# Kernel optimization log

Hardware: AMD Instinct MI355X
Metric: run time of the kernel (lower is better)

## Reference

```python
import jax, jax.numpy as jnp
import numpy as np
from jax import lax

EPS = 1e-5  # BatchNorm eps (torch default)

def _up2_bilinear_ac(x):
    # bilinear upsample x2, align_corners=True; x: [B,C,H,W]
    B, C, H, W = x.shape
    def axis_interp(n_in, n_out):
        pos = jnp.arange(n_out, dtype=jnp.float32) * ((n_in - 1) / (n_out - 1))
        i0 = jnp.floor(pos).astype(jnp.int32)
        i1 = jnp.minimum(i0 + 1, n_in - 1)
        w = (pos - i0.astype(jnp.float32)).astype(x.dtype)
        return i0, i1, w
    i0, i1, wh = axis_interp(H, 2 * H)
    x = x[:, :, i0, :] * (1.0 - wh)[None, None, :, None] + x[:, :, i1, :] * wh[None, None, :, None]
    j0, j1, ww = axis_interp(W, 2 * W)
    x = x[:, :, :, j0] * (1.0 - ww) + x[:, :, :, j1] * ww
    return x

def setup_inputs() -> dict:
    key = jax.random.key(0)
    ks = jax.random.split(key, 8)
    B, Cin, Cout, H, W = 8, 64, 32, 128, 128
    att, K = 16, 2  # attention_channel = max(int(64*0.0625),16)=16; kernel_num=2
    n = lambda k, s, sc: jax.random.normal(k, s, jnp.float32) * sc
    return {
        'x': n(ks[0], (B, Cin, H, W), 1.0),
        'fc_w': n(ks[1], (att, Cin), 0.1),
        'bn_a_gamma': jnp.ones((att,), jnp.float32), 'bn_a_beta': jnp.zeros((att,), jnp.float32),
        'bn_a_mean': jnp.zeros((att,), jnp.float32), 'bn_a_var': jnp.ones((att,), jnp.float32),
        'ch_w': n(ks[2], (Cin, att), 0.1), 'ch_b': jnp.zeros((Cin,), jnp.float32),
        'fil_w': n(ks[3], (Cout, att), 0.1), 'fil_b': jnp.zeros((Cout,), jnp.float32),
        'sp_w': n(ks[4], (9, att), 0.1), 'sp_b': jnp.zeros((9,), jnp.float32),
        'k_w': n(ks[5], (K, att), 0.1), 'k_b': jnp.zeros((K,), jnp.float32),
        'weight': n(ks[6], (K, Cout, Cin, 3, 3), 0.05),
        'bn_gamma': jnp.ones((Cout,), jnp.float32), 'bn_beta': jnp.zeros((Cout,), jnp.float32),
        'bn_mean': jnp.zeros((Cout,), jnp.float32), 'bn_var': jnp.ones((Cout,), jnp.float32),
    }

def reference(x, fc_w, bn_a_gamma, bn_a_beta, bn_a_mean, bn_a_var,
              ch_w, ch_b, fil_w, fil_b, sp_w, sp_b, k_w, k_b,
              weight, bn_gamma, bn_beta, bn_mean, bn_var):
    x = _up2_bilinear_ac(x)
    B, Cin, H, W = x.shape
    K, Cout = weight.shape[0], weight.shape[1]
    # --- ODConv attention branch (on GAP features) ---
    g = x.mean(axis=(2, 3))                                    # [B,Cin]
    h = g @ fc_w.T                                             # [B,att]
    h = (h - bn_a_mean) / jnp.sqrt(bn_a_var + EPS) * bn_a_gamma + bn_a_beta
    h = jax.nn.relu(h)
    ch_att = jax.nn.sigmoid(h @ ch_w.T + ch_b)                 # [B,Cin]
    fil_att = jax.nn.sigmoid(h @ fil_w.T + fil_b)              # [B,Cout]
    sp_att = jax.nn.sigmoid(h @ sp_w.T + sp_b).reshape(B, 1, 1, 1, 3, 3)
    k_att = jax.nn.softmax(h @ k_w.T + k_b, axis=1).reshape(B, K, 1, 1, 1, 1)
    # per-sample aggregated filters: [B,Cout,Cin,3,3]
    agg_w = jnp.sum(k_att * sp_att * weight[None], axis=1)
    # --- dynamic conv (per-sample filter), channel-attended input ---
    x = x * ch_att[:, :, None, None]
    def conv1(xi, wi):
        return lax.conv_general_dilated(xi[None], wi, (1, 1), [(1, 1), (1, 1)],
                                        dimension_numbers=('NCHW', 'OIHW', 'NCHW'))[0]
    y = jax.vmap(conv1)(x, agg_w)                              # [B,Cout,H,W]
    y = y * fil_att[:, :, None, None]
    # --- BatchNorm2d (inference) + GELU (exact erf) ---
    y = (y - bn_mean[:, None, None]) / jnp.sqrt(bn_var[:, None, None] + EPS)
    y = y * bn_gamma[:, None, None] + bn_beta[:, None, None]
    return jax.nn.gelu(y, approximate=False)
```

## Files before the change

kernel.cpp:

```cpp
#include <hip/hip_runtime.h>
#include <hip/hip_bf16.h>

#define EPSBN 1e-5f

typedef short short8 __attribute__((ext_vector_type(8)));
typedef float f32x16 __attribute__((ext_vector_type(16)));

static __device__ __forceinline__ unsigned short f2u(float f){
  __hip_bfloat16 h = __float2bfloat16(f);
  union { __hip_bfloat16 h; unsigned short u; } c; c.h = h; return c.u;
}

#define WS_WR    0
#define WS_G     2048
#define WS_CH    4096
#define WS_SP    6144
#define WS_KA    6656
#define WS_S     7168
#define WS_T     8192
#define WS_AGGB  16384
#define WS_XUP   327680

__global__ void k_wr(float* __restrict__ wr){
  int i = threadIdx.x;
  float s = 0.f;
  for (int r = 0; r < 256; ++r){
    float pos = (float)r * (127.0f/255.0f);
    int i0 = (int)pos; float w = pos - (float)i0; int i1 = min(i0+1,127);
    if (i0 == i) s += 1.0f - w;
    if (i1 == i) s += w;
  }
  wr[i] = s;
}

__global__ void k_gap(const float* __restrict__ x, const float* __restrict__ wr,
                      float* __restrict__ g){
  __shared__ float w[128];
  __shared__ float partial[4];
  int tid = threadIdx.x;
  if (tid < 128) w[tid] = wr[tid];
  __syncthreads();
  const float* xp = x + ((size_t)blockIdx.x << 14);
  float s = 0.f;
  for (int idx = tid; idx < 16384; idx += 256){
    int i = idx >> 7, j = idx & 127;
    s += xp[idx] * w[i] * w[j];
  }
  for (int off = 32; off > 0; off >>= 1) s += __shfl_down(s, off, 64);
  if ((tid & 63) == 0) partial[tid >> 6] = s;
  __syncthreads();
  if (tid == 0) g[blockIdx.x] = (partial[0]+partial[1]+partial[2]+partial[3]) * (1.0f/65536.0f);
}

__global__ void k_att(const float* __restrict__ g,
                      const float* __restrict__ fc_w,
                      const float* __restrict__ bga, const float* __restrict__ bba,
                      const float* __restrict__ bma, const float* __restrict__ bva,
                      const float* __restrict__ ch_w, const float* __restrict__ ch_b,
                      const float* __restrict__ fil_w, const float* __restrict__ fil_b,
                      const float* __restrict__ sp_w, const float* __restrict__ sp_b,
                      const float* __restrict__ k_w, const float* __restrict__ k_b,
                      const float* __restrict__ bn_g, const float* __restrict__ bn_b,
                      const float* __restrict__ bn_m, const float* __restrict__ bn_v,
                      float* __restrict__ ch_att, float* __restrict__ sp_att,
                      float* __restrict__ k_att_o, float* __restrict__ sS, float* __restrict__ tT)
{
  __shared__ float h[8][16];
  int tid = threadIdx.x;
  if (tid < 128){
    int b = tid >> 4, a = tid & 15;
    float acc = 0.f;
    for (int c = 0; c < 64; ++c) acc += g[b*64+c] * fc_w[a*64+c];
    float v = (acc - bma[a]) * rsqrtf(bva[a] + EPSBN) * bga[a] + bba[a];
    h[b][a] = fmaxf(v, 0.f);
  }
  __syncthreads();
  for (int i = tid; i < 512; i += 256){
    int b = i >> 6, c = i & 63;
    float z = ch_b[c];
    for (int a = 0; a < 16; ++a) z += h[b][a]*ch_w[c*16+a];
    ch_att[i] = 1.f/(1.f+expf(-z));
  }
  {
    int b = tid >> 5, o = tid & 31;
    float z = fil_b[o];
    for (int a = 0; a < 16; ++a) z += h[b][a]*fil_w[o*16+a];
    float f = 1.f/(1.f+expf(-z));
    float inv = rsqrtf(bn_v[o] + EPSBN);
    sS[tid] = f * bn_g[o] * inv;
    if (b == 0) tT[o] = bn_b[o] - bn_m[o] * bn_g[o] * inv;
  }
  if (tid < 72){
    int b = tid / 9, s = tid % 9;
    float z = sp_b[s];
    for (int a = 0; a < 16; ++a) z += h[b][a]*sp_w[s*16+a];
    sp_att[tid] = 1.f/(1.f+expf(-z));
  }
  if (tid < 8){
    int b = tid;
    float z0 = k_b[0], z1 = k_b[1];
    for (int a = 0; a < 16; ++a){ z0 += h[b][a]*k_w[a]; z1 += h[b][a]*k_w[16+a]; }
    float m = fmaxf(z0, z1);
    float e0 = expf(z0-m), e1 = expf(z1-m), inv = 1.f/(e0+e1);
    k_att_o[b*2]   = e0*inv;
    k_att_o[b*2+1] = e1*inv;
  }
}

__global__ void k_aggw(const float* __restrict__ weight, const float* __restrict__ ch_att,
                       const float* __restrict__ sp_att, const float* __restrict__ ka,
                       unsigned short* __restrict__ aggb)
{
  int idx = blockIdx.x*256 + threadIdx.x;
  int ci_l = idx & 15;
  int o    = (idx >> 4) & 31;
  int s    = (idx >> 9) % 9;
  int t2   = idx / 4608;
  int cc   = t2 & 3, b = t2 >> 2;
  int ci   = cc*16 + ci_l;
  float w0 = weight[(o*64+ci)*9+s];
  float w1 = weight[((32+o)*64+ci)*9+s];
  float v  = ch_att[b*64+ci] * sp_att[b*9+s] * (ka[b*2]*w0 + ka[b*2+1]*w1);
  aggb[idx] = f2u(v);
}

__global__ __launch_bounds__(256) void k_up(const float* __restrict__ x,
                                            unsigned int* __restrict__ xup32)
{
  __shared__ float xin[16*6*133];
  int tid = threadIdx.x;
  int bi  = blockIdx.x;
  int strip = bi & 31, cc = (bi >> 5) & 3, b = bi >> 7;
  int r0 = strip * 8;
  int i0b = (int)((float)r0 * (127.0f/255.0f));

  for (int e = tid; e < 12288; e += 256){
    int ir = e >> 11;
    int rem = e & 2047;
    int ci = rem >> 7;
    int j  = rem & 127;
    int row = min(i0b + ir, 127);
    xin[ci*798 + ir*133 + j] = x[(((size_t)(b*64 + cc*16 + ci)) << 14) + (row << 7) + j];
  }
  __syncthreads();

  for (int e2 = tid; e2 < 16384; e2 += 256){
    int ci2 = e2 & 7;
    int c   = (e2 >> 3) & 255;
    int rr  = e2 >> 11;
    int r   = r0 + rr;
    float posr = (float)r * (127.0f/255.0f);
    int i0g = (int)posr; float wh = posr - (float)i0g;
    int i1g = min(i0g+1, 127);
    int ir0 = i0g - i0b, ir1 = i1g - i0b;
    float posc = (float)c * (127.0f/255.0f);
    int j0 = (int)posc; float ww = posc - (float)j0;
    int j1 = min(j0+1, 127);
    unsigned int pack = 0;
    #pragma unroll
    for (int u = 0; u < 2; ++u){
      int ci = ci2*2 + u;
      const float* base = &xin[ci*798];
      float v00 = base[ir0*133 + j0], v01 = base[ir0*133 + j1];
      float v10 = base[ir1*133 + j0], v11 = base[ir1*133 + j1];
      float a0 = v00 + (v01 - v00)*ww;
      float a1 = v10 + (v11 - v10)*ww;
      float v  = a0 + (a1 - a0)*wh;
      pack |= ((unsigned int)f2u(v)) << (16*u);
    }
    size_t idx = ((((size_t)(b*4+cc)*256 + r)*256 + c) << 4) + ci2*2;
    xup32[idx >> 1] = pack;
  }
}

__global__ __launch_bounds__(256) void k_conv(const unsigned short* __restrict__ xup,
                                              const unsigned short* __restrict__ aggb,
                                              const float* __restrict__ sS,
                                              const float* __restrict__ tT,
                                              float* __restrict__ out)
{
  __shared__ unsigned short xt[18*18*24];
  __shared__ unsigned short wt[288*24];
  __shared__ float sSs[32], tTs[32];

  int tid = threadIdx.x;
  int bi  = blockIdx.x;
  int b   = bi >> 8, t = bi & 255;
  int p0  = (t >> 4) * 16, q0 = (t & 15) * 16;
  int lane = tid & 63, wv = tid >> 6;
  if (tid < 32){ sSs[tid] = sS[b*32+tid]; tTs[tid] = tT[tid]; }

  f32x16 acc[2];
  #pragma unroll
  for (int i = 0; i < 16; ++i){ acc[0][i] = 0.f; acc[1][i] = 0.f; }

  int n  = lane & 31;
  int kq = lane >> 5;

  for (int cc = 0; cc < 4; ++cc){
    if (cc) __syncthreads();
    for (int e = tid; e < 648; e += 256){
      int rr  = e / 36;
      int rem = e - rr*36;
      int qq  = rem >> 1;
      int half= rem & 1;
      int gr = p0 - 1 + rr, gq = q0 - 1 + qq;
      short8 v = {0,0,0,0,0,0,0,0};
      if ((unsigned)gr < 256u && (unsigned)gq < 256u){
        size_t gidx = ((((size_t)(b*4+cc)*256 + gr)*256 + gq) << 4) + half*8;
        v = *(const short8*)&xup[gidx];
      }
      *(short8*)&xt[(rr*18+qq)*24 + half*8] = v;
    }
    for (int e = tid; e < 576; e += 256){
      int so = e >> 1, half = e & 1;
      size_t gidx = (((size_t)(b*4+cc)*288 + so) << 4) + half*8;
      *(short8*)&wt[so*24 + half*8] = *(const short8*)&aggb[gidx];
    }
    __syncthreads();

    #pragma unroll
    for (int s = 0; s < 9; ++s){
      const int ky = s / 3, kx = s % 3;
      short8 av = *(const short8*)&wt[(s*32 + n)*24 + kq*8];
      #pragma unroll
      for (int tt = 0; tt < 2; ++tt){
        int lr = 2*(2*wv + tt) + (n >> 4);
        int rr = lr + ky;
        int qq = (n & 15) + kx;
        short8 bv = *(const short8*)&xt[(rr*18+qq)*24 + kq*8];
        acc[tt] = __builtin_amdgcn_mfma_f32_32x32x16_bf16(av, bv, acc[tt], 0, 0, 0);
      }
    }
  }

  #pragma unroll
  for (int tt = 0; tt < 2; ++tt){
    int lr = 2*(2*wv + tt) + (n >> 4);
    int p = p0 + lr, q = q0 + (n & 15);
    #pragma unroll
    for (int r = 0; r < 16; ++r){
      int o = (r & 3) + 8*(r >> 2) + 4*kq;
      float val = acc[tt][r]*sSs[o] + tTs[o];
      float gl  = 0.5f*val*(1.f + erff(val*0.70710678118f));
      out[(((size_t)(b*32+o)) << 16) + (p << 8) + q] = gl;
    }
  }
}

extern "C" void kernel_launch(void* const* d_in, const int* in_sizes, int n_in,
                              void* d_out, int out_size, void* d_ws, size_t ws_size,
                              hipStream_t stream)
{
  const float* x     = (const float*)d_in[0];
  const float* fc_w  = (const float*)d_in[1];
  const float* bga   = (const float*)d_in[2];
  const float* bba   = (const float*)d_in[3];
  const float* bma   = (const float*)d_in[4];
  const float* bva   = (const float*)d_in[5];
  const float* ch_w  = (const float*)d_in[6];
  const float* ch_b  = (const float*)d_in[7];
  const float* fil_w = (const float*)d_in[8];
  const float* fil_b = (const float*)d_in[9];
  const float* sp_w  = (const float*)d_in[10];
  const float* sp_b  = (const float*)d_in[11];
  const float* k_w   = (const float*)d_in[12];
  const float* k_b   = (const float*)d_in[13];
  const float* weight= (const float*)d_in[14];
  const float* bn_g  = (const float*)d_in[15];
  const float* bn_b  = (const float*)d_in[16];
  const float* bn_m  = (const float*)d_in[17];
  const float* bn_v  = (const float*)d_in[18];

  char* ws = (char*)d_ws;
  float* wr  = (float*)(ws + WS_WR);
  float* g   = (float*)(ws + WS_G);
  float* ch  = (float*)(ws + WS_CH);
  float* sp  = (float*)(ws + WS_SP);
  float* ka  = (float*)(ws + WS_KA);
  float* sS  = (float*)(ws + WS_S);
  float* tT  = (float*)(ws + WS_T);
  unsigned short* aggb = (unsigned short*)(ws + WS_AGGB);
  unsigned short* xup  = (unsigned short*)(ws + WS_XUP);
  float* out = (float*)d_out;

  hipLaunchKernelGGL(k_wr,   dim3(1),    dim3(128), 0, stream, wr);
  hipLaunchKernelGGL(k_gap,  dim3(512),  dim3(256), 0, stream, x, wr, g);
  hipLaunchKernelGGL(k_att,  dim3(1),    dim3(256), 0, stream, g, fc_w, bga, bba, bma, bva,
                     ch_w, ch_b, fil_w, fil_b, sp_w, sp_b, k_w, k_b,
                     bn_g, bn_b, bn_m, bn_v, ch, sp, ka, sS, tT);
  hipLaunchKernelGGL(k_aggw, dim3(576),  dim3(256), 0, stream, weight, ch, sp, ka, aggb);
  hipLaunchKernelGGL(k_up,   dim3(1024), dim3(256), 0, stream, x, (unsigned int*)xup);
  hipLaunchKernelGGL(k_conv, dim3(2048), dim3(256), 0, stream, xup, aggb, sS, tT, out);
}
```

Baseline: 221.6 us.

## Fuse bilinear upsample into conv tile load and merge attention kernels

Removes the separate upsample kernel and its bf16 upsampled intermediate buffer. Each conv block now loads a small fp32 source tile of x and interpolates its halo tile in shared memory. The attention MLP is recomputed per thread inside the aggregated-weight kernel, and the row-weight computation is folded into the GAP kernel, which now uses float4 loads. This cuts launches from six to three and avoids a large global write and reread. In exchange, every conv block does redundant interpolation work and uses scalar 16-bit LDS stores.

```diff
diff --git a/kernel.cpp b/kernel.cpp
--- a/kernel.cpp
+++ b/kernel.cpp
@@ -11,40 +11,38 @@
   union { __hip_bfloat16 h; unsigned short u; } c; c.h = h; return c.u;
 }
 
-#define WS_WR    0
 #define WS_G     2048
-#define WS_CH    4096
-#define WS_SP    6144
-#define WS_KA    6656
 #define WS_S     7168
 #define WS_T     8192
 #define WS_AGGB  16384
-#define WS_XUP   327680
-
-__global__ void k_wr(float* __restrict__ wr){
-  int i = threadIdx.x;
-  float s = 0.f;
-  for (int r = 0; r < 256; ++r){
-    float pos = (float)r * (127.0f/255.0f);
-    int i0 = (int)pos; float w = pos - (float)i0; int i1 = min(i0+1,127);
-    if (i0 == i) s += 1.0f - w;
-    if (i1 == i) s += w;
-  }
-  wr[i] = s;
-}
-
-__global__ void k_gap(const float* __restrict__ x, const float* __restrict__ wr,
-                      float* __restrict__ g){
+
+__global__ __launch_bounds__(256) void k_gap(const float* __restrict__ x, float* __restrict__ g){
   __shared__ float w[128];
   __shared__ float partial[4];
   int tid = threadIdx.x;
-  if (tid < 128) w[tid] = wr[tid];
+  if (tid < 128){
+    int i = tid;
+    float s = 0.f;
+    int rstart = max(0, (int)floorf((float)(i-1)*(255.0f/127.0f)));
+    #pragma unroll
+    for (int k = 0; k < 8; ++k){
+      int r = rstart + k;
+      if (r <= 255){
+        float pos = (float)r * (127.0f/255.0f);
+        int i0 = (int)pos; float fr = pos - (float)i0; int i1 = min(i0+1,127);
+        if (i0 == i) s += 1.0f - fr;
+        if (i1 == i) s += fr;
+      }
+    }
+    w[i] = s;
+  }
   __syncthreads();
-  const float* xp = x + ((size_t)blockIdx.x << 14);
+  const float4* xp = (const float4*)(x + ((size_t)blockIdx.x << 14));
   float s = 0.f;
-  for (int idx = tid; idx < 16384; idx += 256){
-    int i = idx >> 7, j = idx & 127;
-    s += xp[idx] * w[i] * w[j];
+  for (int gi = tid; gi < 4096; gi += 256){
+    int i = gi >> 5, j4 = (gi & 31) * 4;
+    float4 v = xp[gi];
+    s += (v.x*w[j4] + v.y*w[j4+1] + v.z*w[j4+2] + v.w*w[j4+3]) * w[i];
   }
   for (int off = 32; off > 0; off >>= 1) s += __shfl_down(s, off, 64);
   if ((tid & 63) == 0) partial[tid >> 6] = s;
@@ -52,7 +50,7 @@
   if (tid == 0) g[blockIdx.x] = (partial[0]+partial[1]+partial[2]+partial[3]) * (1.0f/65536.0f);
 }
 
-__global__ void k_att(const float* __restrict__ g,
+__global__ __launch_bounds__(256) void k_aggw(const float* __restrict__ g,
                       const float* __restrict__ fc_w,
                       const float* __restrict__ bga, const float* __restrict__ bba,
                       const float* __restrict__ bma, const float* __restrict__ bva,
@@ -62,8 +60,9 @@
                       const float* __restrict__ k_w, const float* __restrict__ k_b,
                       const float* __restrict__ bn_g, const float* __restrict__ bn_b,
                       const float* __restrict__ bn_m, const float* __restrict__ bn_v,
-                      float* __restrict__ ch_att, float* __restrict__ sp_att,
-                      float* __restrict__ k_att_o, float* __restrict__ sS, float* __restrict__ tT)
+                      const float* __restrict__ weight,
+                      unsigned short* __restrict__ aggb,
+                      float* __restrict__ sS, float* __restrict__ tT)
 {
   __shared__ float h[8][16];
   int tid = threadIdx.x;
@@ -75,105 +74,48 @@
     h[b][a] = fmaxf(v, 0.f);
   }
   __syncthreads();
-  for (int i = tid; i < 512; i += 256){
-    int b = i >> 6, c = i & 63;
-    float z = ch_b[c];
-    for (int a = 0; a < 16; ++a) z += h[b][a]*ch_w[c*16+a];
-    ch_att[i] = 1.f/(1.f+expf(-z));
-  }
-  {
-    int b = tid >> 5, o = tid & 31;
-    float z = fil_b[o];
-    for (int a = 0; a < 16; ++a) z += h[b][a]*fil_w[o*16+a];
-    float f = 1.f/(1.f+expf(-z));
-    float inv = rsqrtf(bn_v[o] + EPSBN);
-    sS[tid] = f * bn_g[o] * inv;
-    if (b == 0) tT[o] = bn_b[o] - bn_m[o] * bn_g[o] * inv;
-  }
-  if (tid < 72){
-    int b = tid / 9, s = tid % 9;
-    float z = sp_b[s];
-    for (int a = 0; a < 16; ++a) z += h[b][a]*sp_w[s*16+a];
-    sp_att[tid] = 1.f/(1.f+expf(-z));
-  }
-  if (tid < 8){
-    int b = tid;
-    float z0 = k_b[0], z1 = k_b[1];
-    for (int a = 0; a < 16; ++a){ z0 += h[b][a]*k_w[a]; z1 += h[b][a]*k_w[16+a]; }
-    float m = fmaxf(z0, z1);
-    float e0 = expf(z0-m), e1 = expf(z1-m), inv = 1.f/(e0+e1);
-    k_att_o[b*2]   = e0*inv;
-    k_att_o[b*2+1] = e1*inv;
-  }
-}
-
-__global__ void k_aggw(const float* __restrict__ weight, const float* __restrict__ ch_att,
-                       const float* __restrict__ sp_att, const float* __restrict__ ka,
-                       unsigned short* __restrict__ aggb)
-{
-  int idx = blockIdx.x*256 + threadIdx.x;
+
+  int idx = blockIdx.x*256 + tid;
   int ci_l = idx & 15;
   int o    = (idx >> 4) & 31;
   int s    = (idx >> 9) % 9;
   int t2   = idx / 4608;
   int cc   = t2 & 3, b = t2 >> 2;
   int ci   = cc*16 + ci_l;
+
+  const float* hb = h[b];
+  float zc = ch_b[ci], zs = sp_b[s];
+  float z0 = k_b[0],  z1 = k_b[1];
+  #pragma unroll
+  for (int a = 0; a < 16; ++a){
+    float hv = hb[a];
+    zc += hv*ch_w[ci*16+a];
+    zs += hv*sp_w[s*16+a];
+    z0 += hv*k_w[a];
+    z1 += hv*k_w[16+a];
+  }
+  float chv = 1.f/(1.f+expf(-zc));
+  float spv = 1.f/(1.f+expf(-zs));
+  float m = fmaxf(z0,z1);
+  float e0 = expf(z0-m), e1 = expf(z1-m), inv = 1.f/(e0+e1);
+  float ka0 = e0*inv, ka1 = e1*inv;
   float w0 = weight[(o*64+ci)*9+s];
   float w1 = weight[((32+o)*64+ci)*9+s];
-  float v  = ch_att[b*64+ci] * sp_att[b*9+s] * (ka[b*2]*w0 + ka[b*2+1]*w1);
-  aggb[idx] = f2u(v);
-}
-
-__global__ __launch_bounds__(256) void k_up(const float* __restrict__ x,
-                                            unsigned int* __restrict__ xup32)
-{
-  __shared__ float xin[16*6*133];
-  int tid = threadIdx.x;
-  int bi  = blockIdx.x;
-  int strip = bi & 31, cc = (bi >> 5) & 3, b = bi >> 7;
-  int r0 = strip * 8;
-  int i0b = (int)((float)r0 * (127.0f/255.0f));
-
-  for (int e = tid; e < 12288; e += 256){
-    int ir = e >> 11;
-    int rem = e & 2047;
-    int ci = rem >> 7;
-    int j  = rem & 127;
-    int row = min(i0b + ir, 127);
-    xin[ci*798 + ir*133 + j] = x[(((size_t)(b*64 + cc*16 + ci)) << 14) + (row << 7) + j];
-  }
-  __syncthreads();
-
-  for (int e2 = tid; e2 < 16384; e2 += 256){
-    int ci2 = e2 & 7;
-    int c   = (e2 >> 3) & 255;
-    int rr  = e2 >> 11;
-    int r   = r0 + rr;
-    float posr = (float)r * (127.0f/255.0f);
-    int i0g = (int)posr; float wh = posr - (float)i0g;
-    int i1g = min(i0g+1, 127);
-    int ir0 = i0g - i0b, ir1 = i1g - i0b;
-    float posc = (float)c * (127.0f/255.0f);
-    int j0 = (int)posc; float ww = posc - (float)j0;
-    int j1 = min(j0+1, 127);
-    unsigned int pack = 0;
-    #pragma unroll
-    for (int u = 0; u < 2; ++u){
-      int ci = ci2*2 + u;
-      const float* base = &xin[ci*798];
-      float v00 = base[ir0*133 + j0], v01 = base[ir0*133 + j1];
-      float v10 = base[ir1*133 + j0], v11 = base[ir1*133 + j1];
-      float a0 = v00 + (v01 - v00)*ww;
-      float a1 = v10 + (v11 - v10)*ww;
-      float v  = a0 + (a1 - a0)*wh;
-      pack |= ((unsigned int)f2u(v)) << (16*u);
-    }
-    size_t idx = ((((size_t)(b*4+cc)*256 + r)*256 + c) << 4) + ci2*2;
-    xup32[idx >> 1] = pack;
-  }
-}
-
-__global__ __launch_bounds__(256) void k_conv(const unsigned short* __restrict__ xup,
+  aggb[idx] = f2u(chv*spv*(ka0*w0 + ka1*w1));
+
+  if (blockIdx.x == 0){
+    int bb = tid >> 5, oo = tid & 31;
+    float z = fil_b[oo];
+    #pragma unroll
+    for (int a = 0; a < 16; ++a) z += h[bb][a]*fil_w[oo*16+a];
+    float f = 1.f/(1.f+expf(-z));
+    float invs = rsqrtf(bn_v[oo] + EPSBN);
+    sS[tid] = f * bn_g[oo] * invs;
+    if (bb == 0) tT[oo] = bn_b[oo] - bn_m[oo]*bn_g[oo]*invs;
+  }
+}
+
+__global__ __launch_bounds__(256) void k_conv(const float* __restrict__ x,
                                               const unsigned short* __restrict__ aggb,
                                               const float* __restrict__ sS,
                                               const float* __restrict__ tT,
@@ -181,6 +123,9 @@
 {
   __shared__ unsigned short xt[18*18*24];
   __shared__ unsigned short wt[288*24];
+  __shared__ float xin[16*121];
+  __shared__ int   ir0s[18], ir1s[18], jc0s[18], jc1s[18];
+  __shared__ float rwhs[18], cwws[18];
   __shared__ float sSs[32], tTs[32];
 
   int tid = threadIdx.x;
@@ -190,6 +135,30 @@
   int lane = tid & 63, wv = tid >> 6;
   if (tid < 32){ sSs[tid] = sS[b*32+tid]; tTs[tid] = tT[tid]; }
 
+  int i0b = (int)((float)max(p0-1,0) * (127.0f/255.0f));
+  int j0b = (int)((float)max(q0-1,0) * (127.0f/255.0f));
+
+  if (tid < 18){
+    int gr = p0 - 1 + tid;
+    if ((unsigned)gr < 256u){
+      float pos = (float)gr * (127.0f/255.0f);
+      int i0 = (int)pos;
+      ir0s[tid] = i0 - i0b;
+      ir1s[tid] = min(i0+1,127) - i0b;
+      rwhs[tid] = pos - (float)i0;
+    } else { ir0s[tid] = -1000; ir1s[tid] = 0; rwhs[tid] = 0.f; }
+  } else if (tid < 36){
+    int k = tid - 18;
+    int gq = q0 - 1 + k;
+    if ((unsigned)gq < 256u){
+      float pos = (float)gq * (127.0f/255.0f);
+      int j0 = (int)pos;
+      jc0s[k] = j0 - j0b;
+      jc1s[k] = min(j0+1,127) - j0b;
+      cwws[k] = pos - (float)j0;
+    } else { jc0s[k] = -1000; jc1s[k] = 0; cwws[k] = 0.f; }
+  }
+
   f32x16 acc[2];
   #pragma unroll
   for (int i = 0; i < 16; ++i){ acc[0][i] = 0.f; acc[1][i] = 0.f; }
@@ -198,24 +167,43 @@
   int kq = lane >> 5;
 
   for (int cc = 0; cc < 4; ++cc){
-    if (cc) __syncthreads();
-    for (int e = tid; e < 648; e += 256){
-      int rr  = e / 36;
-      int rem = e - rr*36;
-      int qq  = rem >> 1;
-      int half= rem & 1;
-      int gr = p0 - 1 + rr, gq = q0 - 1 + qq;
-      short8 v = {0,0,0,0,0,0,0,0};
-      if ((unsigned)gr < 256u && (unsigned)gq < 256u){
-        size_t gidx = ((((size_t)(b*4+cc)*256 + gr)*256 + gq) << 4) + half*8;
-        v = *(const short8*)&xup[gidx];
-      }
-      *(short8*)&xt[(rr*18+qq)*24 + half*8] = v;
+    __syncthreads();
+    {
+      const float* xb = x + (((size_t)(b*64 + cc*16)) << 14);
+      for (int e = tid; e < 1920; e += 256){
+        int ci  = e / 120;
+        int rem = e - ci*120;
+        int ir  = rem / 12;
+        int jj  = rem - ir*12;
+        int row = min(i0b + ir, 127);
+        int col = min(j0b + jj, 127);
+        xin[ci*121 + rem] = xb[((size_t)ci << 14) + (row << 7) + col];
+      }
     }
     for (int e = tid; e < 576; e += 256){
       int so = e >> 1, half = e & 1;
       size_t gidx = (((size_t)(b*4+cc)*288 + so) << 4) + half*8;
       *(short8*)&wt[so*24 + half*8] = *(const short8*)&aggb[gidx];
+    }
+    __syncthreads();
+    for (int e = tid; e < 5184; e += 256){
+      int ci   = e & 15;
+      int rest = e >> 4;
+      int rr   = rest / 18;
+      int qq   = rest - rr*18;
+      unsigned short uv = 0;
+      int i0 = ir0s[rr], j0 = jc0s[qq];
+      if (i0 >= 0 && j0 >= 0){
+        int i1 = ir1s[rr], j1 = jc1s[qq];
+        float wh = rwhs[rr], ww = cwws[qq];
+        const float* base = &xin[ci*121];
+        float v00 = base[i0*12+j0], v01 = base[i0*12+j1];
+        float v10 = base[i1*12+j0], v11 = base[i1*12+j1];
+        float a0 = v00 + (v01 - v00)*ww;
+        float a1 = v10 + (v11 - v10)*ww;
+        uv = f2u(a0 + (a1 - a0)*wh);
+      }
+      xt[(rr*18+qq)*24 + ci] = uv;
     }
     __syncthreads();
 
@@ -273,23 +261,15 @@
   const float* bn_v  = (const float*)d_in[18];
 
   char* ws = (char*)d_ws;
-  float* wr  = (float*)(ws + WS_WR);
   float* g   = (float*)(ws + WS_G);
-  float* ch  = (float*)(ws + WS_CH);
-  float* sp  = (float*)(ws + WS_SP);
-  float* ka  = (float*)(ws + WS_KA);
   float* sS  = (float*)(ws + WS_S);
   float* tT  = (float*)(ws + WS_T);
   unsigned short* aggb = (unsigned short*)(ws + WS_AGGB);
-  unsigned short* xup  = (unsigned short*)(ws + WS_XUP);
   float* out = (float*)d_out;
 
-  hipLaunchKernelGGL(k_wr,   dim3(1),    dim3(128), 0, stream, wr);
-  hipLaunchKernelGGL(k_gap,  dim3(512),  dim3(256), 0, stream, x, wr, g);
-  hipLaunchKernelGGL(k_att,  dim3(1),    dim3(256), 0, stream, g, fc_w, bga, bba, bma, bva,
+  hipLaunchKernelGGL(k_gap,  dim3(512),  dim3(256), 0, stream, x, g);
+  hipLaunchKernelGGL(k_aggw, dim3(576),  dim3(256), 0, stream, g, fc_w, bga, bba, bma, bva,
                      ch_w, ch_b, fil_w, fil_b, sp_w, sp_b, k_w, k_b,
-                     bn_g, bn_b, bn_m, bn_v, ch, sp, ka, sS, tT);
-  hipLaunchKernelGGL(k_aggw, dim3(576),  dim3(256), 0, stream, weight, ch, sp, ka, aggb);
-  hipLaunchKernelGGL(k_up,   dim3(1024), dim3(256), 0, stream, x, (unsigned int*)xup);
-  hipLaunchKernelGGL(k_conv, dim3(2048), dim3(256), 0, stream, xup, aggb, sS, tT, out);
-}
+                     bn_g, bn_b, bn_m, bn_v, weight, aggb, sS, tT);
+  hipLaunchKernelGGL(k_conv, dim3(2048), dim3(256), 0, stream, x, aggb, sS, tT, out);
+}
```

Result: faster. 206.9 us (-6.7%).
